# Optimization experiments

Hardware: AMD Instinct MI355X
Metric: run time of the kernel (lower is better)

Reference implementation:

```python
import jax, jax.numpy as jnp
import numpy as np

NUM_HEADS = 8
TOPK = 100


def setup_inputs() -> dict:
    key = jax.random.key(0)
    ks = jax.random.split(key, 8)
    B, N, C = 2, 2048, 512
    q = jax.random.normal(ks[0], (B, N, C), dtype=jnp.float32)
    k = jax.random.normal(ks[1], (B, N, C), dtype=jnp.float32)
    v = jax.random.normal(ks[2], (B, N, C), dtype=jnp.float32)
    w_scale = 0.02
    Wq = jax.random.normal(ks[3], (C, C), dtype=jnp.float32) * w_scale
    Wk = jax.random.normal(ks[4], (C, C), dtype=jnp.float32) * w_scale
    Wv = jax.random.normal(ks[5], (C, C), dtype=jnp.float32) * w_scale
    Wp = jax.random.normal(ks[6], (C, C), dtype=jnp.float32) * w_scale
    bq = jnp.zeros((C,), jnp.float32)
    bk = jnp.zeros((C,), jnp.float32)
    bv = jnp.zeros((C,), jnp.float32)
    bp = jnp.zeros((C,), jnp.float32)
    return {"q": q, "k": k, "v": v, "Wq": Wq, "bq": bq, "Wk": Wk, "bk": bk,
            "Wv": Wv, "bv": bv, "Wp": Wp, "bp": bp}


def reference(q, k, v, Wq, bq, Wk, bk, Wv, bv, Wp, bp):
    B, N, C = q.shape
    H = NUM_HEADS
    D = C // H
    scale = D ** (-0.5)
    # per-head projections: [B, N, C] -> [B, H, N, D]
    qh = (q @ Wq.T + bq).reshape(B, N, H, D).transpose(0, 2, 1, 3)
    kh = (k @ Wk.T + bk).reshape(B, N, H, D).transpose(0, 2, 1, 3)
    vh = (v @ Wv.T + bv).reshape(B, N, H, D).transpose(0, 2, 1, 3)
    # dense scores [B, H, N, N]
    attn = jnp.einsum("bhnd,bhmd->bhnm", qh, kh) * scale
    # top-k mask: equivalent to torch scatter of topk indices (ties are
    # measure-zero for continuous scores). Keep only the topk largest per row.
    top_vals = jax.lax.top_k(attn, TOPK)[0]          # [B, H, N, TOPK]
    thresh = top_vals[..., -1:]                      # k-th largest per row
    attn = jnp.where(attn >= thresh, attn, -jnp.inf)
    attn = jax.nn.softmax(attn, axis=-1)
    out = jnp.einsum("bhnm,bhmd->bhnd", attn, vh)
    out = out.transpose(0, 2, 1, 3).reshape(B, N, C)
    return out @ Wp.T + bp
```

## Files before the change

kernel.cpp:

```cpp
#include <hip/hip_runtime.h>
#include <stdint.h>

#define B_ 2
#define N_ 2048
#define C_ 512
#define H_ 8
#define D_ 64
#define TOPK_ 100
#define BN_ (B_*N_)
#define CAP_ 256

typedef __attribute__((ext_vector_type(8))) short s16x8;
typedef __attribute__((ext_vector_type(4))) float f32x4;

__device__ __forceinline__ int mbcnt64(unsigned long long m) {
  return __builtin_amdgcn_mbcnt_hi((unsigned)(m >> 32),
         __builtin_amdgcn_mbcnt_lo((unsigned)m, 0u));
}
__device__ __forceinline__ float u2f(unsigned uu) {
  unsigned bits = (uu & 0x80000000u) ? (uu ^ 0x80000000u) : ~uu;
  return __uint_as_float(bits);
}
__device__ __forceinline__ unsigned short bf16rn(float x) {
  unsigned u = __float_as_uint(x);
  unsigned r = (u + 0x7fffu + ((u >> 16) & 1u)) >> 16;
  return (unsigned short)r;
}
__device__ __forceinline__ float bf16f(unsigned short h) {
  return __uint_as_float(((unsigned)h) << 16);
}
__device__ __forceinline__ void split3(float x, unsigned short& h,
                                       unsigned short& m, unsigned short& l) {
  h = bf16rn(x);
  float r1 = x - bf16f(h);
  m = bf16rn(r1);
  float r2 = r1 - bf16f(m);
  l = bf16rn(r2);
}
#define SWZ(r, sl) (((sl) ^ (((r) >> 1) & 3)) << 3)
#define MFMA_BF16(a, b, c) __builtin_amdgcn_mfma_f32_16x16x32_bf16(a, b, c, 0, 0, 0)
#define SIX_PASS(acc, ah, am, al, bh, bm, bl) \
  do { \
    acc = MFMA_BF16(ah, bl, acc); \
    acc = MFMA_BF16(am, bm, acc); \
    acc = MFMA_BF16(al, bh, acc); \
    acc = MFMA_BF16(ah, bm, acc); \
    acc = MFMA_BF16(am, bh, acc); \
    acc = MFMA_BF16(ah, bh, acc); \
  } while (0)

__global__ __launch_bounds__(256)
void wsplit(const float* __restrict__ W0, const float* __restrict__ W1,
            unsigned short* __restrict__ Wsp)
{
  int z = blockIdx.y;
  const float* W = (z == 0) ? W0 : W1;
  const size_t WN = (size_t)C_ * C_;
  unsigned short* Wh = Wsp + (size_t)z * 3 * WN;
  unsigned short* Wm = Wh + WN;
  unsigned short* Wl = Wh + 2 * WN;
  int i = blockIdx.x * 256 + threadIdx.x;
  unsigned short h, m, l;
  split3(W[i], h, m, l);
  Wh[i] = h; Wm[i] = m; Wl[i] = l;
}

__global__ __launch_bounds__(256)
void gemm64(const float* __restrict__ X0, const float* __restrict__ X1,
            const float* __restrict__ W0, const float* __restrict__ W1,
            const float* __restrict__ b0, const float* __restrict__ b1,
            float* __restrict__ O0, float* __restrict__ O1)
{
  int z = blockIdx.z;
  const float* X = (z == 0) ? X0 : X1;
  const float* W = (z == 0) ? W0 : W1;
  const float* bs = (z == 0) ? b0 : b1;
  float* O = (z == 0) ? O0 : O1;

  __shared__ float Xs[32][68];
  __shared__ float Ws[32][68];

  int t = threadIdx.x;
  int tr = t >> 4, tc = t & 15;
  int m0 = blockIdx.x * 64, c0 = blockIdx.y * 64;

  float acc[4][4] = {};

  for (int k0 = 0; k0 < C_; k0 += 32) {
    #pragma unroll
    for (int j2 = 0; j2 < 2; ++j2) {
      int fid = t + j2 * 256;
      int row = fid >> 3;
      int dk  = (fid & 7) << 2;
      float4 xv = *(const float4*)(X + (size_t)(m0 + row) * C_ + k0 + dk);
      Xs[dk+0][row] = xv.x; Xs[dk+1][row] = xv.y; Xs[dk+2][row] = xv.z; Xs[dk+3][row] = xv.w;
      float4 wv = *(const float4*)(W + (size_t)(c0 + row) * C_ + k0 + dk);
      Ws[dk+0][row] = wv.x; Ws[dk+1][row] = wv.y; Ws[dk+2][row] = wv.z; Ws[dk+3][row] = wv.w;
    }
    __syncthreads();
    #pragma unroll
    for (int k = 0; k < 32; ++k) {
      float4 a = *(const float4*)&Xs[k][tr << 2];
      float4 b = *(const float4*)&Ws[k][tc << 2];
      float ar[4] = {a.x, a.y, a.z, a.w};
      float br[4] = {b.x, b.y, b.z, b.w};
      #pragma unroll
      for (int i = 0; i < 4; ++i)
        #pragma unroll
        for (int j = 0; j < 4; ++j)
          acc[i][j] = fmaf(ar[i], br[j], acc[i][j]);
    }
    __syncthreads();
  }

  float bv[4];
  #pragma unroll
  for (int j = 0; j < 4; ++j) bv[j] = bs[c0 + (tc << 2) + j];

  #pragma unroll
  for (int i = 0; i < 4; ++i) {
    float4 o = make_float4(acc[i][0] + bv[0], acc[i][1] + bv[1],
                           acc[i][2] + bv[2], acc[i][3] + bv[3]);
    int m = m0 + (tr << 2) + i;
    int bb = m >> 11;
    int tok = m & (N_ - 1);
    int h = blockIdx.y;
    *(float4*)(O + (((size_t)(bb * H_ + h) * N_) + tok) * D_ + (tc << 2)) = o;
  }
}

__global__ __launch_bounds__(256)
void gemm_mfma(const float* __restrict__ A,
               const unsigned short* __restrict__ Wplanes,
               const float* __restrict__ bias,
               float* __restrict__ O, int scatter)
{
  const size_t WN = (size_t)C_ * C_;
  const unsigned short* Wh = Wplanes;
  const unsigned short* Wm = Wplanes + WN;
  const unsigned short* Wl = Wplanes + 2 * WN;

  __shared__ unsigned short Ah[128][32], Am[128][32], Al[128][32];
  __shared__ unsigned short Bh[64][32],  Bm[64][32],  Bl[64][32];

  int t = threadIdx.x;
  int l = t & 63, wv = t >> 6;
  int wm = wv >> 1, wn = wv & 1;
  int m0 = blockIdx.x * 128, n0 = blockIdx.y * 64;

  f32x4 acc[4][2];
  #pragma unroll
  for (int i = 0; i < 4; ++i)
    #pragma unroll
    for (int j = 0; j < 2; ++j) acc[i][j] = (f32x4){0.f,0.f,0.f,0.f};

  for (int k0 = 0; k0 < C_; k0 += 32) {
    #pragma unroll
    for (int sj = 0; sj < 2; ++sj) {
      int s = t + sj * 256;
      int r = s >> 2, sl = s & 3, c = sl << 3;
      int co = SWZ(r, sl);
      const float* src = A + (size_t)(m0 + r) * C_ + k0 + c;
      float4 x0 = *(const float4*)src;
      float4 x1 = *(const float4*)(src + 4);
      float xs[8] = {x0.x,x0.y,x0.z,x0.w,x1.x,x1.y,x1.z,x1.w};
      unsigned short hv[8], mv[8], lv[8];
      #pragma unroll
      for (int j = 0; j < 8; ++j) split3(xs[j], hv[j], mv[j], lv[j]);
      *(s16x8*)&Ah[r][co] = *(s16x8*)hv;
      *(s16x8*)&Am[r][co] = *(s16x8*)mv;
      *(s16x8*)&Al[r][co] = *(s16x8*)lv;
    }
    {
      int r = t >> 2, sl = t & 3, c = sl << 3;
      int co = SWZ(r, sl);
      size_t boff = (size_t)(n0 + r) * C_ + k0 + c;
      *(s16x8*)&Bh[r][co] = *(const s16x8*)&Wh[boff];
      *(s16x8*)&Bm[r][co] = *(const s16x8*)&Wm[boff];
      *(s16x8*)&Bl[r][co] = *(const s16x8*)&Wl[boff];
    }
    __syncthreads();

    int lr = l & 15, s0 = l >> 4;
    s16x8 ah[4], am[4], al[4];
    #pragma unroll
    for (int mi = 0; mi < 4; ++mi) {
      int R = wm*64 + mi*16 + lr;
      int co = SWZ(R, s0);
      ah[mi] = *(const s16x8*)&Ah[R][co];
      am[mi] = *(const s16x8*)&Am[R][co];
      al[mi] = *(const s16x8*)&Al[R][co];
    }
    #pragma unroll
    for (int nj = 0; nj < 2; ++nj) {
      int Rb = wn*32 + nj*16 + lr;
      int co = SWZ(Rb, s0);
      s16x8 bh = *(const s16x8*)&Bh[Rb][co];
      s16x8 bm = *(const s16x8*)&Bm[Rb][co];
      s16x8 bl = *(const s16x8*)&Bl[Rb][co];
      #pragma unroll
      for (int mi = 0; mi < 4; ++mi)
        SIX_PASS(acc[mi][nj], ah[mi], am[mi], al[mi], bh, bm, bl);
    }
    __syncthreads();
  }

  int lr = l & 15, lq = l >> 4;
  #pragma unroll
  for (int mi = 0; mi < 4; ++mi) {
    #pragma unroll
    for (int nj = 0; nj < 2; ++nj) {
      #pragma unroll
      for (int r = 0; r < 4; ++r) {
        int m = m0 + wm*64 + mi*16 + lq*4 + r;
        int c = n0 + wn*32 + nj*16 + lr;
        float y = acc[mi][nj][r] + bias[c];
        if (scatter) {
          int bb = m >> 11, tok = m & (N_ - 1);
          int hh = c >> 6, d = c & 63;
          O[(((size_t)(bb * H_ + hh) * N_) + tok) * D_ + d] = y;
        } else {
          O[(size_t)m * C_ + c] = y;
        }
      }
    }
  }
}

__global__ __launch_bounds__(256)
void qk128(const float* __restrict__ qh, const float* __restrict__ kh,
           float* __restrict__ S, int slice0, int row0, int Rrows)
{
  int z = blockIdx.z;
  int slice = slice0 + z;
  const float* Q = qh + (size_t)slice * N_ * D_;
  const float* K = kh + (size_t)slice * N_ * D_;
  float* Sp = S + (size_t)z * Rrows * N_;

  __shared__ float Qs[32][132];
  __shared__ float Ks[32][132];

  int t = threadIdx.x;
  int tr = t >> 4, tc = t & 15;
  int n0 = blockIdx.x * 128, m0 = blockIdx.y * 128;

  float acc[2][2][4][4] = {};

  #pragma unroll
  for (int k0 = 0; k0 < D_; k0 += 32) {
    #pragma unroll
    for (int jj = 0; jj < 4; ++jj) {
      int fid = t + jj * 256;
      int row = fid >> 3;
      int dk  = (fid & 7) << 2;
      float4 qv = *(const float4*)(Q + (size_t)(row0 + n0 + row) * D_ + k0 + dk);
      Qs[dk+0][row] = qv.x; Qs[dk+1][row] = qv.y; Qs[dk+2][row] = qv.z; Qs[dk+3][row] = qv.w;
      float4 kv = *(const float4*)(K + (size_t)(m0 + row) * D_ + k0 + dk);
      Ks[dk+0][row] = kv.x; Ks[dk+1][row] = kv.y; Ks[dk+2][row] = kv.z; Ks[dk+3][row] = kv.w;
    }
    __syncthreads();
    #pragma unroll 8
    for (int k = 0; k < 32; ++k) {
      float a[2][4], b[2][4];
      *(float4*)&a[0][0] = *(const float4*)&Qs[k][tr << 2];
      *(float4*)&a[1][0] = *(const float4*)&Qs[k][64 + (tr << 2)];
      *(float4*)&b[0][0] = *(const float4*)&Ks[k][tc << 2];
      *(float4*)&b[1][0] = *(const float4*)&Ks[k][64 + (tc << 2)];
      #pragma unroll
      for (int ia = 0; ia < 2; ++ia)
        #pragma unroll
        for (int ib = 0; ib < 2; ++ib)
          #pragma unroll
          for (int i = 0; i < 4; ++i)
            #pragma unroll
            for (int j = 0; j < 4; ++j)
              acc[ia][ib][i][j] = fmaf(a[ia][i], b[ib][j], acc[ia][ib][i][j]);
    }
    __syncthreads();
  }

  const float scale = 0.125f;
  #pragma unroll
  for (int ia = 0; ia < 2; ++ia)
    #pragma unroll
    for (int i = 0; i < 4; ++i) {
      int n = n0 + ia*64 + (tr << 2) + i;
      #pragma unroll
      for (int ib = 0; ib < 2; ++ib) {
        float4 o = make_float4(acc[ia][ib][i][0] * scale, acc[ia][ib][i][1] * scale,
                               acc[ia][ib][i][2] * scale, acc[ia][ib][i][3] * scale);
        *(float4*)(Sp + (size_t)n * N_ + m0 + ib*64 + (tc << 2)) = o;
      }
    }
}

__global__ __launch_bounds__(256)
void topk_softmax_pv(const float* __restrict__ S, const float* __restrict__ vh,
                     float* __restrict__ outp, int slice0, int row0, int log2R)
{
  __shared__ float wL[4][CAP_];
  __shared__ unsigned short iL[4][CAP_];

  int t = threadIdx.x;
  int wv = t >> 6;
  int lane = t & 63;
  int gr = blockIdx.x * 4 + wv;
  int s_local = gr >> log2R;
  int rrow = gr & ((1 << log2R) - 1);
  int slice = slice0 + s_local;
  int row = row0 + rrow;

  const float* Srow = S + ((size_t)gr) * N_;

  unsigned u[32];
  #pragma unroll
  for (int i = 0; i < 8; ++i) {
    float4 v = *(const float4*)(Srow + i * 256 + lane * 4);
    float xv[4] = {v.x, v.y, v.z, v.w};
    #pragma unroll
    for (int c = 0; c < 4; ++c) {
      unsigned bits = __float_as_uint(xv[c]);
      u[i*4+c] = bits ^ ((unsigned)(((int)bits) >> 31) | 0x80000000u);
    }
  }

  unsigned thr = 0u;
  for (int bit = 31; bit >= 0; --bit) {
    unsigned cand = thr | (1u << bit);
    int c = 0;
    #pragma unroll
    for (int i = 0; i < 32; ++i) c += (u[i] >= cand) ? 1 : 0;
    #pragma unroll
    for (int off = 32; off >= 1; off >>= 1) c += __shfl_xor(c, off);
    if (c >= TOPK_) {
      thr = cand;
      if (c == TOPK_) break;
    }
  }

  unsigned mxu = 0u;
  #pragma unroll
  for (int i = 0; i < 32; ++i) mxu = (u[i] > mxu) ? u[i] : mxu;
  #pragma unroll
  for (int off = 32; off >= 1; off >>= 1) {
    unsigned o = (unsigned)__shfl_xor((int)mxu, off);
    mxu = (o > mxu) ? o : mxu;
  }
  float mx = u2f(mxu);

  float s = 0.f;
  #pragma unroll
  for (int i = 0; i < 32; ++i) {
    bool kp = (u[i] >= thr);
    float ev = kp ? __expf(u2f(u[i]) - mx) : 0.f;
    s += ev;
  }
  #pragma unroll
  for (int off = 32; off >= 1; off >>= 1) s += __shfl_xor(s, off);
  float inv = 1.f / s;

  int base = 0;
  #pragma unroll
  for (int i = 0; i < 32; ++i) {
    bool kp = (u[i] >= thr);
    unsigned long long m = __ballot(kp);
    if (kp) {
      int pos = base + mbcnt64(m);
      if (pos < CAP_) {
        wL[wv][pos] = __expf(u2f(u[i]) - mx) * inv;
        iL[wv][pos] = (unsigned short)(((i >> 2) << 8) + (lane << 2) + (i & 3));
      }
    }
    base += __popcll(m);
  }
  int total = base < CAP_ ? base : CAP_;

  const float* Vs = vh + (size_t)slice * N_ * D_;
  float a0=0.f,a1=0.f,a2=0.f,a3=0.f,a4=0.f,a5=0.f,a6=0.f,a7=0.f;
  int e = 0;
  for (; e + 8 <= total; e += 8) {
    float w0=wL[wv][e+0], w1=wL[wv][e+1], w2=wL[wv][e+2], w3=wL[wv][e+3];
    float w4=wL[wv][e+4], w5=wL[wv][e+5], w6=wL[wv][e+6], w7=wL[wv][e+7];
    int j0=iL[wv][e+0], j1=iL[wv][e+1], j2=iL[wv][e+2], j3=iL[wv][e+3];
    int j4=iL[wv][e+4], j5=iL[wv][e+5], j6=iL[wv][e+6], j7=iL[wv][e+7];
    float v0=Vs[(size_t)j0*D_+lane], v1=Vs[(size_t)j1*D_+lane];
    float v2=Vs[(size_t)j2*D_+lane], v3=Vs[(size_t)j3*D_+lane];
    float v4=Vs[(size_t)j4*D_+lane], v5=Vs[(size_t)j5*D_+lane];
    float v6=Vs[(size_t)j6*D_+lane], v7=Vs[(size_t)j7*D_+lane];
    a0 = fmaf(w0, v0, a0); a1 = fmaf(w1, v1, a1);
    a2 = fmaf(w2, v2, a2); a3 = fmaf(w3, v3, a3);
    a4 = fmaf(w4, v4, a4); a5 = fmaf(w5, v5, a5);
    a6 = fmaf(w6, v6, a6); a7 = fmaf(w7, v7, a7);
  }
  for (; e < total; ++e)
    a0 = fmaf(wL[wv][e], Vs[(size_t)iL[wv][e] * D_ + lane], a0);
  float acc = ((a0 + a1) + (a2 + a3)) + ((a4 + a5) + (a6 + a7));

  int b = slice >> 3;
  int h = slice & 7;
  outp[((size_t)(b * N_ + row)) * C_ + h * D_ + lane] = acc;
}

extern "C" void kernel_launch(void* const* d_in, const int* in_sizes, int n_in,
                              void* d_out, int out_size, void* d_ws, size_t ws_size,
                              hipStream_t stream) {
  const float* q  = (const float*)d_in[0];
  const float* k  = (const float*)d_in[1];
  const float* v  = (const float*)d_in[2];
  const float* Wq = (const float*)d_in[3];
  const float* bq = (const float*)d_in[4];
  const float* Wk = (const float*)d_in[5];
  const float* bk = (const float*)d_in[6];
  const float* Wv = (const float*)d_in[7];
  const float* bv = (const float*)d_in[8];
  const float* Wp = (const float*)d_in[9];
  const float* bp = (const float*)d_in[10];

  const size_t NB = (size_t)B_ * H_ * N_ * D_;
  const size_t WN = (size_t)C_ * C_;
  float* qh  = (float*)d_ws;
  float* kh  = qh + NB;
  float* vh  = kh + NB;
  float* pre = vh + NB;
  unsigned short* Wsp = (unsigned short*)(pre + NB);
  float* S   = (float*)(Wsp + 2 * 3 * WN);

  size_t fixedB = 4 * NB * 4 + 2 * 3 * WN * 2;
  size_t sliceB = (size_t)N_ * N_ * 4;
  size_t avail = (ws_size > fixedB) ? ws_size - fixedB : 0;

  int ns = 1, R = 2048;
  if      (avail >= 8 * sliceB) { ns = 8; R = 2048; }
  else if (avail >= 4 * sliceB) { ns = 4; R = 2048; }
  else if (avail >= 2 * sliceB) { ns = 2; R = 2048; }
  else if (avail >= 1 * sliceB) { ns = 1; R = 2048; }
  else if (avail >= sliceB / 2) { ns = 1; R = 1024; }
  else                          { ns = 1; R = 512;  }
  int log2R = (R == 2048) ? 11 : ((R == 1024) ? 10 : 9);

  dim3 blk(256);

  wsplit<<<dim3(WN / 256, 2), blk, 0, stream>>>(Wv, Wp, Wsp);

  gemm64<<<dim3(BN_/64, C_/64, 2), blk, 0, stream>>>(
      q, k, Wq, Wk, bq, bk, qh, kh);

  gemm_mfma<<<dim3(BN_/128, C_/64), blk, 0, stream>>>(
      v, Wsp, bv, vh, 1);

  for (int s0 = 0; s0 < B_ * H_; s0 += ns) {
    int cur = (B_ * H_ - s0) < ns ? (B_ * H_ - s0) : ns;
    for (int r0 = 0; r0 < N_; r0 += R) {
      qk128<<<dim3(R/128, N_/128, cur), blk, 0, stream>>>(qh, kh, S, s0, r0, R);
      topk_softmax_pv<<<dim3(cur * (R/4)), blk, 0, stream>>>(S, vh, pre, s0, r0, log2R);
    }
  }

  gemm_mfma<<<dim3(BN_/128, C_/64), blk, 0, stream>>>(
      pre, Wsp + 3 * WN, bp, (float*)d_out, 0);
}
```

Baseline: 379.6 us.

## Enlarge Q/K projection tile, skip threshold bits, fuse softmax normalization, widen slice batching

The Q/K projection GEMM now computes a 128x64 tile per block (8x4 per thread) and XOR-swizzles its shared-memory layout to cut bank conflicts. The top-k kernel computes the row max first and skips radix threshold bits above it. It also merges the exp-sum pass into the compaction pass and applies the 1/sum normalization once after the PV accumulation. The PV loop reads weights and indices with vector LDS loads, and up to 16 slices can be batched per launch when the workspace allows. Register pressure rises in the GEMM, and the deferred normalization slightly changes rounding.

```diff
diff --git a/kernel.cpp b/kernel.cpp
--- a/kernel.cpp
+++ b/kernel.cpp
@@ -11,6 +11,7 @@
 #define CAP_ 256
 
 typedef __attribute__((ext_vector_type(8))) short s16x8;
+typedef __attribute__((ext_vector_type(8))) unsigned short u16x8;
 typedef __attribute__((ext_vector_type(4))) float f32x4;
 
 __device__ __forceinline__ int mbcnt64(unsigned long long m) {
@@ -66,10 +67,10 @@
 }
 
 __global__ __launch_bounds__(256)
-void gemm64(const float* __restrict__ X0, const float* __restrict__ X1,
-            const float* __restrict__ W0, const float* __restrict__ W1,
-            const float* __restrict__ b0, const float* __restrict__ b1,
-            float* __restrict__ O0, float* __restrict__ O1)
+void gemm_qkproj(const float* __restrict__ X0, const float* __restrict__ X1,
+                 const float* __restrict__ W0, const float* __restrict__ W1,
+                 const float* __restrict__ b0, const float* __restrict__ b1,
+                 float* __restrict__ O0, float* __restrict__ O1)
 {
   int z = blockIdx.z;
   const float* X = (z == 0) ? X0 : X1;
@@ -77,38 +78,49 @@
   const float* bs = (z == 0) ? b0 : b1;
   float* O = (z == 0) ? O0 : O1;
 
-  __shared__ float Xs[32][68];
-  __shared__ float Ws[32][68];
+  __shared__ float Xs[32][128];
+  __shared__ float Ws[32][64];
 
   int t = threadIdx.x;
   int tr = t >> 4, tc = t & 15;
-  int m0 = blockIdx.x * 64, c0 = blockIdx.y * 64;
-
-  float acc[4][4] = {};
+  int m0 = blockIdx.x * 128, c0 = blockIdx.y * 64;
+
+  float acc[8][4] = {};
 
   for (int k0 = 0; k0 < C_; k0 += 32) {
     #pragma unroll
-    for (int j2 = 0; j2 < 2; ++j2) {
-      int fid = t + j2 * 256;
+    for (int j = 0; j < 4; ++j) {
+      int fid = t + j * 256;
       int row = fid >> 3;
       int dk  = (fid & 7) << 2;
+      int co  = row ^ (dk & 24);
       float4 xv = *(const float4*)(X + (size_t)(m0 + row) * C_ + k0 + dk);
-      Xs[dk+0][row] = xv.x; Xs[dk+1][row] = xv.y; Xs[dk+2][row] = xv.z; Xs[dk+3][row] = xv.w;
-      float4 wv = *(const float4*)(W + (size_t)(c0 + row) * C_ + k0 + dk);
-      Ws[dk+0][row] = wv.x; Ws[dk+1][row] = wv.y; Ws[dk+2][row] = wv.z; Ws[dk+3][row] = wv.w;
+      Xs[dk+0][co] = xv.x; Xs[dk+1][co] = xv.y;
+      Xs[dk+2][co] = xv.z; Xs[dk+3][co] = xv.w;
+    }
+    #pragma unroll
+    for (int j = 0; j < 2; ++j) {
+      int fid = t + j * 256;
+      int cc = fid >> 3;
+      int dk = (fid & 7) << 2;
+      int co = cc ^ (dk & 24);
+      float4 wv = *(const float4*)(W + (size_t)(c0 + cc) * C_ + k0 + dk);
+      Ws[dk+0][co] = wv.x; Ws[dk+1][co] = wv.y;
+      Ws[dk+2][co] = wv.z; Ws[dk+3][co] = wv.w;
     }
     __syncthreads();
     #pragma unroll
     for (int k = 0; k < 32; ++k) {
-      float4 a = *(const float4*)&Xs[k][tr << 2];
-      float4 b = *(const float4*)&Ws[k][tc << 2];
-      float ar[4] = {a.x, a.y, a.z, a.w};
-      float br[4] = {b.x, b.y, b.z, b.w};
-      #pragma unroll
-      for (int i = 0; i < 4; ++i)
+      int swz = k & 24;
+      float a[8], b[4];
+      *(float4*)&a[0] = *(const float4*)&Xs[k][(tr << 3) ^ swz];
+      *(float4*)&a[4] = *(const float4*)&Xs[k][((tr << 3) + 4) ^ swz];
+      *(float4*)&b[0] = *(const float4*)&Ws[k][(tc << 2) ^ swz];
+      #pragma unroll
+      for (int i = 0; i < 8; ++i)
         #pragma unroll
         for (int j = 0; j < 4; ++j)
-          acc[i][j] = fmaf(ar[i], br[j], acc[i][j]);
+          acc[i][j] = fmaf(a[i], b[j], acc[i][j]);
     }
     __syncthreads();
   }
@@ -118,10 +130,10 @@
   for (int j = 0; j < 4; ++j) bv[j] = bs[c0 + (tc << 2) + j];
 
   #pragma unroll
-  for (int i = 0; i < 4; ++i) {
+  for (int i = 0; i < 8; ++i) {
+    int m = m0 + (tr << 3) + i;
     float4 o = make_float4(acc[i][0] + bv[0], acc[i][1] + bv[1],
                            acc[i][2] + bv[2], acc[i][3] + bv[3]);
-    int m = m0 + (tr << 2) + i;
     int bb = m >> 11;
     int tok = m & (N_ - 1);
     int h = blockIdx.y;
@@ -324,9 +336,21 @@
     }
   }
 
+  unsigned mxu = 0u;
+  #pragma unroll
+  for (int i = 0; i < 32; ++i) mxu = (u[i] > mxu) ? u[i] : mxu;
+  #pragma unroll
+  for (int off = 32; off >= 1; off >>= 1) {
+    unsigned o = (unsigned)__shfl_xor((int)mxu, off);
+    mxu = (o > mxu) ? o : mxu;
+  }
+  unsigned mxs = (unsigned)__builtin_amdgcn_readfirstlane((int)mxu);
+  float mx = u2f(mxs);
+
   unsigned thr = 0u;
   for (int bit = 31; bit >= 0; --bit) {
     unsigned cand = thr | (1u << bit);
+    if (cand > mxs) continue;
     int c = 0;
     #pragma unroll
     for (int i = 0; i < 32; ++i) c += (u[i] >= cand) ? 1 : 0;
@@ -338,63 +362,47 @@
     }
   }
 
-  unsigned mxu = 0u;
-  #pragma unroll
-  for (int i = 0; i < 32; ++i) mxu = (u[i] > mxu) ? u[i] : mxu;
-  #pragma unroll
-  for (int off = 32; off >= 1; off >>= 1) {
-    unsigned o = (unsigned)__shfl_xor((int)mxu, off);
-    mxu = (o > mxu) ? o : mxu;
-  }
-  float mx = u2f(mxu);
-
   float s = 0.f;
-  #pragma unroll
-  for (int i = 0; i < 32; ++i) {
-    bool kp = (u[i] >= thr);
-    float ev = kp ? __expf(u2f(u[i]) - mx) : 0.f;
-    s += ev;
-  }
-  #pragma unroll
-  for (int off = 32; off >= 1; off >>= 1) s += __shfl_xor(s, off);
-  float inv = 1.f / s;
-
   int base = 0;
   #pragma unroll
   for (int i = 0; i < 32; ++i) {
     bool kp = (u[i] >= thr);
     unsigned long long m = __ballot(kp);
+    float ev = kp ? __expf(u2f(u[i]) - mx) : 0.f;
+    s += ev;
     if (kp) {
       int pos = base + mbcnt64(m);
       if (pos < CAP_) {
-        wL[wv][pos] = __expf(u2f(u[i]) - mx) * inv;
+        wL[wv][pos] = ev;
         iL[wv][pos] = (unsigned short)(((i >> 2) << 8) + (lane << 2) + (i & 3));
       }
     }
     base += __popcll(m);
   }
+  #pragma unroll
+  for (int off = 32; off >= 1; off >>= 1) s += __shfl_xor(s, off);
+  float inv = 1.f / s;
   int total = base < CAP_ ? base : CAP_;
 
   const float* Vs = vh + (size_t)slice * N_ * D_;
   float a0=0.f,a1=0.f,a2=0.f,a3=0.f,a4=0.f,a5=0.f,a6=0.f,a7=0.f;
   int e = 0;
   for (; e + 8 <= total; e += 8) {
-    float w0=wL[wv][e+0], w1=wL[wv][e+1], w2=wL[wv][e+2], w3=wL[wv][e+3];
-    float w4=wL[wv][e+4], w5=wL[wv][e+5], w6=wL[wv][e+6], w7=wL[wv][e+7];
-    int j0=iL[wv][e+0], j1=iL[wv][e+1], j2=iL[wv][e+2], j3=iL[wv][e+3];
-    int j4=iL[wv][e+4], j5=iL[wv][e+5], j6=iL[wv][e+6], j7=iL[wv][e+7];
-    float v0=Vs[(size_t)j0*D_+lane], v1=Vs[(size_t)j1*D_+lane];
-    float v2=Vs[(size_t)j2*D_+lane], v3=Vs[(size_t)j3*D_+lane];
-    float v4=Vs[(size_t)j4*D_+lane], v5=Vs[(size_t)j5*D_+lane];
-    float v6=Vs[(size_t)j6*D_+lane], v7=Vs[(size_t)j7*D_+lane];
-    a0 = fmaf(w0, v0, a0); a1 = fmaf(w1, v1, a1);
-    a2 = fmaf(w2, v2, a2); a3 = fmaf(w3, v3, a3);
-    a4 = fmaf(w4, v4, a4); a5 = fmaf(w5, v5, a5);
-    a6 = fmaf(w6, v6, a6); a7 = fmaf(w7, v7, a7);
+    float4 wa = *(const float4*)&wL[wv][e];
+    float4 wb = *(const float4*)&wL[wv][e+4];
+    u16x8 jj = *(const u16x8*)&iL[wv][e];
+    float v0=Vs[(size_t)jj[0]*D_+lane], v1=Vs[(size_t)jj[1]*D_+lane];
+    float v2=Vs[(size_t)jj[2]*D_+lane], v3=Vs[(size_t)jj[3]*D_+lane];
+    float v4=Vs[(size_t)jj[4]*D_+lane], v5=Vs[(size_t)jj[5]*D_+lane];
+    float v6=Vs[(size_t)jj[6]*D_+lane], v7=Vs[(size_t)jj[7]*D_+lane];
+    a0 = fmaf(wa.x, v0, a0); a1 = fmaf(wa.y, v1, a1);
+    a2 = fmaf(wa.z, v2, a2); a3 = fmaf(wa.w, v3, a3);
+    a4 = fmaf(wb.x, v4, a4); a5 = fmaf(wb.y, v5, a5);
+    a6 = fmaf(wb.z, v6, a6); a7 = fmaf(wb.w, v7, a7);
   }
   for (; e < total; ++e)
     a0 = fmaf(wL[wv][e], Vs[(size_t)iL[wv][e] * D_ + lane], a0);
-  float acc = ((a0 + a1) + (a2 + a3)) + ((a4 + a5) + (a6 + a7));
+  float acc = (((a0 + a1) + (a2 + a3)) + ((a4 + a5) + (a6 + a7))) * inv;
 
   int b = slice >> 3;
   int h = slice & 7;
@@ -430,19 +438,20 @@
   size_t avail = (ws_size > fixedB) ? ws_size - fixedB : 0;
 
   int ns = 1, R = 2048;
-  if      (avail >= 8 * sliceB) { ns = 8; R = 2048; }
-  else if (avail >= 4 * sliceB) { ns = 4; R = 2048; }
-  else if (avail >= 2 * sliceB) { ns = 2; R = 2048; }
-  else if (avail >= 1 * sliceB) { ns = 1; R = 2048; }
-  else if (avail >= sliceB / 2) { ns = 1; R = 1024; }
-  else                          { ns = 1; R = 512;  }
+  if      (avail >= 16 * sliceB) { ns = 16; R = 2048; }
+  else if (avail >= 8 * sliceB)  { ns = 8;  R = 2048; }
+  else if (avail >= 4 * sliceB)  { ns = 4;  R = 2048; }
+  else if (avail >= 2 * sliceB)  { ns = 2;  R = 2048; }
+  else if (avail >= 1 * sliceB)  { ns = 1;  R = 2048; }
+  else if (avail >= sliceB / 2)  { ns = 1;  R = 1024; }
+  else                           { ns = 1;  R = 512;  }
   int log2R = (R == 2048) ? 11 : ((R == 1024) ? 10 : 9);
 
   dim3 blk(256);
 
   wsplit<<<dim3(WN / 256, 2), blk, 0, stream>>>(Wv, Wp, Wsp);
 
-  gemm64<<<dim3(BN_/64, C_/64, 2), blk, 0, stream>>>(
+  gemm_qkproj<<<dim3(BN_/128, C_/64, 2), blk, 0, stream>>>(
       q, k, Wq, Wk, bq, bk, qh, kh);
 
   gemm_mfma<<<dim3(BN_/128, C_/64), blk, 0, stream>>>(
```

Measured after the change: 372.6 us, median of 2. No clear change (-1.8%).
